# Kernel optimization log

Hardware: AMD Instinct MI355X
Metric: run time of the kernel (lower is better)

## Reference

```python
import jax, jax.numpy as jnp
import numpy as np

EMBED_DIM = 256
NUM_EMBEDDINGS = 1024
COMMITMENT_COST = 0.25


def setup_inputs() -> dict:
    key = jax.random.key(0)
    k1, k2 = jax.random.split(key)
    z_e = jax.random.normal(k1, (64, 32, 32, EMBED_DIM), dtype=jnp.float32)
    # variance_scaling(fan_in, uniform) ~ U(-sqrt(3/fan_in), sqrt(3/fan_in))
    lim = float(np.sqrt(3.0 / EMBED_DIM))
    codebook = jax.random.uniform(k2, (NUM_EMBEDDINGS, EMBED_DIM), dtype=jnp.float32,
                                  minval=-lim, maxval=lim)
    return {"z_e": z_e, "codebook": codebook}


def reference(z_e, codebook):
    codebook = jnp.asarray(codebook, dtype=jnp.float32)
    z_flat = jnp.reshape(z_e, (-1, codebook.shape[1]))  # [N, D]
    # ||z||^2 - 2 z.c + ||c||^2 -> [N, K]
    distances = (jnp.sum(z_flat ** 2, axis=1, keepdims=True)
                 - 2.0 * jnp.dot(z_flat, codebook.T)
                 + jnp.sum(codebook ** 2, axis=1))
    encoding_indices = jnp.argmin(distances, axis=1)  # [N]
    quantized = jnp.reshape(codebook[encoding_indices], z_e.shape)
    commitment_loss = COMMITMENT_COST * jnp.mean((jax.lax.stop_gradient(quantized) - z_e) ** 2)
    embedding_loss = jnp.mean((quantized - jax.lax.stop_gradient(z_e)) ** 2)
    quantized = z_e + jax.lax.stop_gradient(quantized - z_e)  # straight-through
    return (quantized, commitment_loss, embedding_loss, encoding_indices)
```

## Files before the change

### kernel.cpp

```cpp
#include <hip/hip_runtime.h>

#define NROWS  65536
#define DIM    256
#define KCB    1024
#define DELTA  0.012f
#define DELTA2 2.0e-4f
#define NRMAX  65536

typedef __attribute__((ext_vector_type(8))) _Float16 v8h;
typedef __attribute__((ext_vector_type(4))) float v4f;
typedef __attribute__((ext_vector_type(4))) int   v4i;

__device__ __forceinline__ unsigned short h16(float x) {
  _Float16 h = (_Float16)x;
  return __builtin_bit_cast(unsigned short, h);
}
__device__ __forceinline__ unsigned pk2h(float a, float b) {
  return (unsigned)h16(a) | ((unsigned)h16(b) << 16);
}
__device__ __forceinline__ v4i pk8h(float4 a, float4 b) {
  v4i r; r.x = (int)pk2h(a.x,a.y); r.y = (int)pk2h(a.z,a.w);
  r.z = (int)pk2h(b.x,b.y); r.w = (int)pk2h(b.z,b.w);
  return r;
}
__device__ __forceinline__ float f16f(float x) { return (float)(_Float16)x; }
__device__ __forceinline__ void gld16(const void* g, void* l) {
  __builtin_amdgcn_global_load_lds(
      (const __attribute__((address_space(1))) unsigned int*)g,
      (__attribute__((address_space(3))) unsigned int*)l, 16, 0, 0);
}

__global__ __launch_bounds__(256) void prep_kernel(const float* __restrict__ cb,
                                                   float* __restrict__ cnorm,
                                                   unsigned short* __restrict__ cbh,
                                                   unsigned short* __restrict__ cbl,
                                                   int* __restrict__ cnt,
                                                   int* __restrict__ cnt2) {
  int g = blockIdx.x * 256 + threadIdx.x;
  if (g == 0) { *cnt = 0; *cnt2 = 0; }
  int k = g >> 2, q = g & 3;
  int nt = k >> 7, c = k & 127;
  const float4* row = reinterpret_cast<const float4*>(cb + (size_t)k * DIM) + q * 16;
  size_t off = (size_t)((nt * 4 + q) * 128 + c) * 64;
  unsigned short* dh = cbh + off;
  unsigned short* dl = cbl + off;
  int xr = (c & 7) << 3;
  double s = 0.0;
#pragma unroll
  for (int i = 0; i < 8; ++i) {
    float4 a = row[2 * i], b = row[2 * i + 1];
    s += (double)a.x * a.x + (double)a.y * a.y + (double)a.z * a.z + (double)a.w * a.w;
    s += (double)b.x * b.x + (double)b.y * b.y + (double)b.z * b.z + (double)b.w * b.w;
    *(v4i*)(dh + ((i * 8) ^ xr)) = pk8h(a, b);
    float4 ar, br;
    ar.x = a.x - f16f(a.x); ar.y = a.y - f16f(a.y);
    ar.z = a.z - f16f(a.z); ar.w = a.w - f16f(a.w);
    br.x = b.x - f16f(b.x); br.y = b.y - f16f(b.y);
    br.z = b.z - f16f(b.z); br.w = b.w - f16f(b.w);
    *(v4i*)(dl + ((i * 8) ^ xr)) = pk8h(ar, br);
  }
  s += __shfl_xor(s, 1);
  s += __shfl_xor(s, 2);
  if (q == 0) cnorm[k] = (float)s;
}

__global__ __launch_bounds__(256, 2) void vq_mfma(
    const float* __restrict__ z, const unsigned short* __restrict__ cbh,
    const float* __restrict__ cnw, int* __restrict__ idx_arr,
    int* __restrict__ list, int* __restrict__ cnt) {
  __shared__ __align__(16) short S[32768];

  const int t = threadIdx.x;
  const int l = t & 63;
  const int w = t >> 6;
  const int l15 = l & 15, lhi = l >> 4;
  const int wm = w * 32;
  const int r0 = blockIdx.x * 128;

#pragma unroll
  for (int p = 0; p < 16; ++p) {
    int u = t + p * 256;
    int row = u >> 5, k8 = u & 31;
    const float4* s = (const float4*)(z + (size_t)(r0 + row) * DIM + k8 * 8);
    float4 a = s[0], b = s[1];
    *(v4i*)(S + row * 256 + ((k8 * 8) ^ ((row & 7) << 3))) = pk8h(a, b);
  }
  __syncthreads();

  v8h A[2][8];
#pragma unroll
  for (int mf = 0; mf < 2; ++mf) {
    int arow = wm + mf * 16 + l15;
    int base = arow * 256, xr = (arow & 7) << 3;
#pragma unroll
    for (int ks8 = 0; ks8 < 8; ++ks8)
      A[mf][ks8] = *(const v8h*)(S + base + ((ks8 * 32 + lhi * 8) ^ xr));
  }
  __syncthreads();

  auto stageC = [&](int p) {
    const char* gb = (const char*)cbh + (size_t)p * 32768 + w * 8192 + l * 16;
    char* lb = (char*)(S + (p & 1) * 16384) + w * 8192;
#pragma unroll
    for (int j = 0; j < 8; ++j) gld16(gb + j * 1024, lb + j * 1024);
  };

  int bcode[8], boff[8], bxr[8];
#pragma unroll
  for (int nf = 0; nf < 8; ++nf) {
    bcode[nf] = nf * 16 + l15;
    boff[nf] = bcode[nf] * 64;
    bxr[nf] = (bcode[nf] & 7) << 3;
  }

  float m1[8], m2[8]; int i1[8];
#pragma unroll
  for (int sl = 0; sl < 8; ++sl) { m1[sl] = 3.0e38f; m2[sl] = 3.0e38f; i1[sl] = 0; }

  stageC(0);
  __syncthreads();

  for (int nt = 0; nt < 8; ++nt) {
    float cnv[8];
#pragma unroll
    for (int nf = 0; nf < 8; ++nf) cnv[nf] = cnw[nt * 128 + bcode[nf]];

    v4f acc[2][8];
#pragma unroll
    for (int mf = 0; mf < 2; ++mf)
#pragma unroll
      for (int nf = 0; nf < 8; ++nf) acc[mf][nf] = (v4f){0.f, 0.f, 0.f, 0.f};

    for (int kh = 0; kh < 2; ++kh) {
      int p = nt * 2 + kh;
      if (p < 15) stageC(p + 1);
      const short* cur = S + (p & 1) * 16384;
#pragma unroll
      for (int ks = 0; ks < 4; ++ks) {
        int sub = (ks >> 1) * 8192;
        int ko = (ks & 1) * 32 + lhi * 8;
        v8h b[8];
#pragma unroll
        for (int nf = 0; nf < 8; ++nf)
          b[nf] = *(const v8h*)(cur + sub + boff[nf] + (ko ^ bxr[nf]));
#pragma unroll
        for (int mf = 0; mf < 2; ++mf)
#pragma unroll
          for (int nf = 0; nf < 8; ++nf)
            acc[mf][nf] = __builtin_amdgcn_mfma_f32_16x16x32_f16(A[mf][kh * 4 + ks], b[nf], acc[mf][nf], 0, 0, 0);
      }
      __syncthreads();
    }

#pragma unroll
    for (int mf = 0; mf < 2; ++mf)
#pragma unroll
      for (int nf = 0; nf < 8; ++nf) {
        int code = nt * 128 + bcode[nf];
#pragma unroll
        for (int r = 0; r < 4; ++r) {
          float s = fmaf(-2.f, acc[mf][nf][r], cnv[nf]);
          int sl = mf * 4 + r;
          m2[sl] = fminf(m2[sl], fmaxf(m1[sl], s));
          bool lt = s < m1[sl];
          i1[sl] = lt ? code : i1[sl];
          m1[sl] = lt ? s : m1[sl];
        }
      }
  }

#pragma unroll
  for (int off = 1; off < 16; off <<= 1) {
#pragma unroll
    for (int sl = 0; sl < 8; ++sl) {
      float o1 = __shfl_xor(m1[sl], off);
      int   oi = __shfl_xor(i1[sl], off);
      float o2 = __shfl_xor(m2[sl], off);
      bool bb = (o1 < m1[sl]) || (o1 == m1[sl] && oi < i1[sl]);
      float hi = fmaxf(m1[sl], o1);
      m2[sl] = fminf(hi, fminf(m2[sl], o2));
      m1[sl] = bb ? o1 : m1[sl];
      i1[sl] = bb ? oi : i1[sl];
    }
  }

  if (l15 == 0) {
#pragma unroll
    for (int sl = 0; sl < 8; ++sl) {
      int row = wm + (sl >> 2) * 16 + lhi * 4 + (sl & 3);
      idx_arr[r0 + row] = i1[sl];
      if (m2[sl] - m1[sl] < DELTA) {
        int p = atomicAdd(cnt, 1);
        list[p] = r0 + row;
      }
    }
  }
}

__global__ __launch_bounds__(256, 1) void vq_refine(
    const float* __restrict__ z,
    const unsigned short* __restrict__ cbh, const unsigned short* __restrict__ cbl,
    const float* __restrict__ cnw, const int* __restrict__ list,
    const int* __restrict__ cnt,
    float* __restrict__ pm1, float* __restrict__ pm2, int* __restrict__ pi1) {
  __shared__ __align__(16) short Ch[2][8192];
  __shared__ __align__(16) short Cl[2][8192];
  __shared__ int rows_s[64];

  const int t = threadIdx.x;
  const int l = t & 63, w = t >> 6;
  const int l15 = l & 15, lhi = l >> 4;
  const int n = *cnt;
  const int ngroups = (n + 63) >> 6;
  const int cq = blockIdx.x & 3;

  auto stage2 = [&](int g, int buf) {
    size_t go = (size_t)g * 16384 + w * 4096 + l * 16;
    char* lh = (char*)Ch[buf] + w * 4096;
    char* ll = (char*)Cl[buf] + w * 4096;
#pragma unroll
    for (int j = 0; j < 4; ++j) gld16((const char*)cbh + go + j * 1024, lh + j * 1024);
#pragma unroll
    for (int j = 0; j < 4; ++j) gld16((const char*)cbl + go + j * 1024, ll + j * 1024);
  };

  const int bxr = (l15 & 7) << 3;

  for (int grp = blockIdx.x >> 2; grp < ngroups; grp += (gridDim.x >> 2)) {
    int base = grp * 64;
    __syncthreads();
    if (t < 64) rows_s[t] = list[min(base + t, n - 1)];
    __syncthreads();
    int rowg = rows_s[w * 16 + l15];

    v8h Ah[8], Al[8];
#pragma unroll
    for (int ks8 = 0; ks8 < 8; ++ks8) {
      const float* p = z + (size_t)rowg * 256 + ks8 * 32 + lhi * 8;
      float4 a = *(const float4*)p, b = *(const float4*)(p + 4);
      v8h hv, lv;
      hv[0] = (_Float16)a.x; lv[0] = (_Float16)(a.x - (float)hv[0]);
      hv[1] = (_Float16)a.y; lv[1] = (_Float16)(a.y - (float)hv[1]);
      hv[2] = (_Float16)a.z; lv[2] = (_Float16)(a.z - (float)hv[2]);
      hv[3] = (_Float16)a.w; lv[3] = (_Float16)(a.w - (float)hv[3]);
      hv[4] = (_Float16)b.x; lv[4] = (_Float16)(b.x - (float)hv[4]);
      hv[5] = (_Float16)b.y; lv[5] = (_Float16)(b.y - (float)hv[5]);
      hv[6] = (_Float16)b.z; lv[6] = (_Float16)(b.z - (float)hv[6]);
      hv[7] = (_Float16)b.w; lv[7] = (_Float16)(b.w - (float)hv[7]);
      Ah[ks8] = hv; Al[ks8] = lv;
    }

    stage2(cq * 8, 0);
    __syncthreads();

    float m1[4], m2[4]; int i1[4];
#pragma unroll
    for (int r = 0; r < 4; ++r) { m1[r] = 3.0e38f; m2[r] = 3.0e38f; i1[r] = 0; }

#pragma unroll
    for (int tnt = 0; tnt < 2; ++tnt) {
      int nt = cq * 2 + tnt;
      float cnv[8];
#pragma unroll
      for (int nf = 0; nf < 8; ++nf) cnv[nf] = cnw[nt * 128 + nf * 16 + l15];

      v4f acc[8];
#pragma unroll
      for (int nf = 0; nf < 8; ++nf) acc[nf] = (v4f){0.f, 0.f, 0.f, 0.f};

      for (int kc = 0; kc < 4; ++kc) {
        int ph = tnt * 4 + kc;
        int g = nt * 4 + kc;
        if (ph < 7) stage2(g + 1, (ph + 1) & 1);
        const short* ch = Ch[ph & 1];
        const short* cl = Cl[ph & 1];
#pragma unroll
        for (int ks = 0; ks < 2; ++ks) {
          int ko = (ks * 32 + lhi * 8) ^ bxr;
          v8h bh[8], bl8[8];
#pragma unroll
          for (int nf = 0; nf < 8; ++nf) {
            int bo = (nf * 16 + l15) * 64 + ko;
            bh[nf]  = *(const v8h*)(ch + bo);
            bl8[nf] = *(const v8h*)(cl + bo);
          }
          v8h ah = Ah[kc * 2 + ks], al = Al[kc * 2 + ks];
#pragma unroll
          for (int nf = 0; nf < 8; ++nf) {
            acc[nf] = __builtin_amdgcn_mfma_f32_16x16x32_f16(al, bh[nf], acc[nf], 0, 0, 0);
            acc[nf] = __builtin_amdgcn_mfma_f32_16x16x32_f16(ah, bl8[nf], acc[nf], 0, 0, 0);
            acc[nf] = __builtin_amdgcn_mfma_f32_16x16x32_f16(ah, bh[nf], acc[nf], 0, 0, 0);
          }
        }
        __syncthreads();
      }

#pragma unroll
      for (int nf = 0; nf < 8; ++nf) {
        int code = nt * 128 + nf * 16 + l15;
#pragma unroll
        for (int r = 0; r < 4; ++r) {
          float s = fmaf(-2.f, acc[nf][r], cnv[nf]);
          m2[r] = fminf(m2[r], fmaxf(m1[r], s));
          bool lt = s < m1[r];
          i1[r] = lt ? code : i1[r];
          m1[r] = lt ? s : m1[r];
        }
      }
    }

#pragma unroll
    for (int off = 1; off < 16; off <<= 1) {
#pragma unroll
      for (int r = 0; r < 4; ++r) {
        float o1 = __shfl_xor(m1[r], off);
        int   oi = __shfl_xor(i1[r], off);
        float o2 = __shfl_xor(m2[r], off);
        bool bb = (o1 < m1[r]) || (o1 == m1[r] && oi < i1[r]);
        float hi = fmaxf(m1[r], o1);
        m2[r] = fminf(hi, fminf(m2[r], o2));
        m1[r] = bb ? o1 : m1[r];
        i1[r] = bb ? oi : i1[r];
      }
    }

    if (l15 == 0) {
#pragma unroll
      for (int r = 0; r < 4; ++r) {
        int fr = w * 16 + lhi * 4 + r;
        int pos = base + fr;
        if (pos < n) {
          pm1[cq * NRMAX + pos] = m1[r];
          pm2[cq * NRMAX + pos] = m2[r];
          pi1[cq * NRMAX + pos] = i1[r];
        }
      }
    }
  }
}

__global__ __launch_bounds__(256) void vq_merge(
    const int* __restrict__ list, const int* __restrict__ cnt,
    const float* __restrict__ pm1, const float* __restrict__ pm2,
    const int* __restrict__ pi1, int* __restrict__ idx_arr,
    int* __restrict__ list2, int* __restrict__ cnt2) {
  int i = blockIdx.x * 256 + threadIdx.x;
  int n = *cnt;
  if (i >= n) return;
  float m1 = pm1[i], m2 = pm2[i];
  int   i1 = pi1[i];
#pragma unroll
  for (int cq = 1; cq < 4; ++cq) {
    float o1 = pm1[cq * NRMAX + i];
    float o2 = pm2[cq * NRMAX + i];
    int   oi = pi1[cq * NRMAX + i];
    bool bb = (o1 < m1) || (o1 == m1 && oi < i1);
    float hi = fmaxf(m1, o1);
    m2 = fminf(hi, fminf(m2, o2));
    m1 = bb ? o1 : m1;
    i1 = bb ? oi : i1;
  }
  int row = list[i];
  idx_arr[row] = i1;
  if (m2 - m1 < DELTA2) {
    int p = atomicAdd(cnt2, 1);
    list2[p] = row;
  }
}

__global__ __launch_bounds__(256) void vq_rescue(
    const float* __restrict__ z, const float* __restrict__ cb,
    const float* __restrict__ cnw, const int* __restrict__ list,
    const int* __restrict__ cnt, int* __restrict__ idx_arr) {
  __shared__ float zs[256];
  __shared__ float As;
  __shared__ float wmin[4];
  __shared__ int   widx[4];

  const int t = threadIdx.x;
  const int l = t & 63, w = t >> 6;
  const int n = *cnt;

  for (int i = blockIdx.x; i < n; i += gridDim.x) {
    int row = list[i];
    __syncthreads();
    if (t < 64) ((float4*)zs)[t] = ((const float4*)(z + (size_t)row * DIM))[t];
    __syncthreads();
    if (t < 4) {
      double s = 0.0;
      const float* zz = zs + t * 64;
      for (int d = 0; d < 64; ++d) { float v = zz[d]; s += (double)v * v; }
      s += __shfl_xor(s, 1);
      s += __shfl_xor(s, 2);
      if (t == 0) As = (float)s;
    }
    __syncthreads();
    float Af = As;

    const float4* c0 = (const float4*)(cb + (size_t)(t      ) * DIM);
    const float4* c1 = (const float4*)(cb + (size_t)(t + 256) * DIM);
    const float4* c2 = (const float4*)(cb + (size_t)(t + 512) * DIM);
    const float4* c3 = (const float4*)(cb + (size_t)(t + 768) * DIM);
    float a0 = 0.f, a1 = 0.f, a2 = 0.f, a3 = 0.f;
    for (int d4 = 0; d4 < 64; ++d4) {
      float4 zq = *(const float4*)(zs + d4 * 4);
      float4 va = c0[d4], vb = c1[d4], vc = c2[d4], vd = c3[d4];
      a0 = fmaf(zq.x, va.x, a0); a0 = fmaf(zq.y, va.y, a0);
      a0 = fmaf(zq.z, va.z, a0); a0 = fmaf(zq.w, va.w, a0);
      a1 = fmaf(zq.x, vb.x, a1); a1 = fmaf(zq.y, vb.y, a1);
      a1 = fmaf(zq.z, vb.z, a1); a1 = fmaf(zq.w, vb.w, a1);
      a2 = fmaf(zq.x, vc.x, a2); a2 = fmaf(zq.y, vc.y, a2);
      a2 = fmaf(zq.z, vc.z, a2); a2 = fmaf(zq.w, vc.w, a2);
      a3 = fmaf(zq.x, vd.x, a3); a3 = fmaf(zq.y, vd.y, a3);
      a3 = fmaf(zq.z, vd.z, a3); a3 = fmaf(zq.w, vd.w, a3);
    }
    float accs[4] = {a0, a1, a2, a3};
    float mv = 3.0e38f; int mi = 0;
#pragma unroll
    for (int j = 0; j < 4; ++j) {
      int code = t + j * 256;
      float t1 = fmaf(-2.f, accs[j], Af);
      float t2 = t1 + cnw[code];
      if (t2 < mv) { mv = t2; mi = code; }
    }
#pragma unroll
    for (int off = 1; off < 64; off <<= 1) {
      float ov = __shfl_xor(mv, off);
      int   oi = __shfl_xor(mi, off);
      if (ov < mv || (ov == mv && oi < mi)) { mv = ov; mi = oi; }
    }
    if (l == 0) { wmin[w] = mv; widx[w] = mi; }
    __syncthreads();
    if (t == 0) {
      float bm = wmin[0]; int bi = widx[0];
#pragma unroll
      for (int q = 1; q < 4; ++q)
        if (wmin[q] < bm || (wmin[q] == bm && widx[q] < bi)) { bm = wmin[q]; bi = widx[q]; }
      idx_arr[row] = bi;
    }
    __syncthreads();
  }
}

__global__ __launch_bounds__(256) void vq_epilogue(
    const float* __restrict__ z, const float* __restrict__ cb,
    const int* __restrict__ idx_arr, float* __restrict__ out_q,
    float* __restrict__ out_idx, double* __restrict__ partial) {
  __shared__ int idxs[16];
  __shared__ double lw[4];
  const int t = threadIdx.x;
  const int b0 = blockIdx.x * 16;
  if (t < 16) {
    int k = idx_arr[b0 + t];
    idxs[t] = k;
    out_idx[b0 + t] = (float)k;
  }
  __syncthreads();
  const float4* zb = (const float4*)(z + (size_t)b0 * DIM);
  float4* qb = (float4*)(out_q + (size_t)b0 * DIM);
  double ls = 0.0;
#pragma unroll
  for (int p = 0; p < 4; ++p) {
    int fi = p * 256 + t;
    int ki = idxs[fi >> 6];
    float4 zv = zb[fi];
    float4 cv = ((const float4*)(cb + (size_t)ki * DIM))[fi & 63];
    float dx = cv.x - zv.x, dy = cv.y - zv.y, dz = cv.z - zv.z, dw = cv.w - zv.w;
    float4 o; o.x = zv.x + dx; o.y = zv.y + dy; o.z = zv.z + dz; o.w = zv.w + dw;
    qb[fi] = o;
    ls += (double)dx * dx + (double)dy * dy + (double)dz * dz + (double)dw * dw;
  }
#pragma unroll
  for (int off = 1; off < 64; off <<= 1) ls += __shfl_xor(ls, off);
  if ((t & 63) == 0) lw[t >> 6] = ls;
  __syncthreads();
  if (t == 0) partial[blockIdx.x] = lw[0] + lw[1] + lw[2] + lw[3];
}

__global__ __launch_bounds__(256) void finalize_kernel(const double* __restrict__ partial,
                                                       float* __restrict__ out_losses) {
  __shared__ double lw[4];
  const int t = threadIdx.x;
  double s = 0.0;
  for (int i = t; i < 4096; i += 256) s += partial[i];
#pragma unroll
  for (int off = 1; off < 64; off <<= 1) s += __shfl_xor(s, off);
  if ((t & 63) == 0) lw[t >> 6] = s;
  __syncthreads();
  if (t == 0) {
    double mse = (lw[0] + lw[1] + lw[2] + lw[3]) / ((double)NROWS * (double)DIM);
    out_losses[0] = (float)(0.25 * mse);
    out_losses[1] = (float)mse;
  }
}

extern "C" void kernel_launch(void* const* d_in, const int* in_sizes, int n_in,
                              void* d_out, int out_size, void* d_ws, size_t ws_size,
                              hipStream_t stream) {
  const float* z  = (const float*)d_in[0];
  const float* cb = (const float*)d_in[1];
  float* out = (float*)d_out;

  char* ws = (char*)d_ws;
  int*            cnt     = (int*)(ws + 0);
  int*            cnt2    = (int*)(ws + 8);
  float*          cnorm   = (float*)(ws + 4096);
  double*         partial = (double*)(ws + 8192);
  int*            idx_arr = (int*)(ws + 40960);
  int*            list    = (int*)(ws + 303104);
  int*            list2   = (int*)(ws + 565248);
  unsigned short* cbh     = (unsigned short*)(ws + 827392);
  unsigned short* cbl     = (unsigned short*)(ws + 1351680);
  float*          pm1     = (float*)(ws + 1875968);
  float*          pm2     = (float*)(ws + 2924544);
  int*            pi1     = (int*)(ws + 3973120);

  float* out_q      = out;
  float* out_losses = out + 16777216;
  float* out_idx    = out + 16777218;

  prep_kernel<<<16, 256, 0, stream>>>(cb, cnorm, cbh, cbl, cnt, cnt2);
  vq_mfma<<<NROWS / 128, 256, 0, stream>>>(z, cbh, cnorm, idx_arr, list, cnt);
  vq_refine<<<1024, 256, 0, stream>>>(z, cbh, cbl, cnorm, list, cnt, pm1, pm2, pi1);
  vq_merge<<<NRMAX / 256, 256, 0, stream>>>(list, cnt, pm1, pm2, pi1, idx_arr, list2, cnt2);
  vq_rescue<<<256, 256, 0, stream>>>(z, cb, cnorm, list2, cnt2, idx_arr);
  vq_epilogue<<<NROWS / 16, 256, 0, stream>>>(z, cb, idx_arr, out_q, out_idx, partial);
  finalize_kernel<<<1, 256, 0, stream>>>(partial, out_losses);
}
```

Before: 145.6 us.

## Triple-buffer codebook staging with finer chunks and single barrier per step

Replaces the double-buffered codebook staging (32KB chunks, two syncthreads per step) with a three-slot ring of 16KB chunks, prefetched two steps ahead. Each step is guarded by an explicit vmcnt wait plus one s_barrier. Codebook norms are preloaded into shared memory once instead of read from global memory each tile. The aim is to hide global-to-LDS latency and cut barrier stalls. In exchange it adds more LDS usage and relies on hand-written waitcnt counts matching the number of outstanding loads.

```diff
diff --git a/kernel.cpp b/kernel.cpp
--- a/kernel.cpp
+++ b/kernel.cpp
@@ -96,13 +96,20 @@
     for (int ks8 = 0; ks8 < 8; ++ks8)
       A[mf][ks8] = *(const v8h*)(S + base + ((ks8 * 32 + lhi * 8) ^ xr));
   }
+  float cn4[4];
+#pragma unroll
+  for (int j = 0; j < 4; ++j) cn4[j] = cnw[t + j * 256];
   __syncthreads();
 
-  auto stageC = [&](int p) {
-    const char* gb = (const char*)cbh + (size_t)p * 32768 + w * 8192 + l * 16;
-    char* lb = (char*)(S + (p & 1) * 16384) + w * 8192;
-#pragma unroll
-    for (int j = 0; j < 8; ++j) gld16(gb + j * 1024, lb + j * 1024);
+  float* CNS = (float*)(S + 24576);
+#pragma unroll
+  for (int j = 0; j < 4; ++j) CNS[t + j * 256] = cn4[j];
+
+  auto stageC = [&](int g) {
+    const char* gb = (const char*)cbh + (size_t)g * 16384 + w * 4096 + l * 16;
+    char* lb = (char*)S + (g % 3) * 16384 + w * 4096 + l * 16;
+#pragma unroll
+    for (int j = 0; j < 4; ++j) gld16(gb + j * 1024, lb + j * 1024);
   };
 
   int bcode[8], boff[8], bxr[8];
@@ -117,39 +124,38 @@
 #pragma unroll
   for (int sl = 0; sl < 8; ++sl) { m1[sl] = 3.0e38f; m2[sl] = 3.0e38f; i1[sl] = 0; }
 
-  stageC(0);
   __syncthreads();
+  stageC(0); stageC(1);
+
+  v4f acc[2][8];
 
   for (int nt = 0; nt < 8; ++nt) {
-    float cnv[8];
-#pragma unroll
-    for (int nf = 0; nf < 8; ++nf) cnv[nf] = cnw[nt * 128 + bcode[nf]];
-
-    v4f acc[2][8];
 #pragma unroll
     for (int mf = 0; mf < 2; ++mf)
 #pragma unroll
       for (int nf = 0; nf < 8; ++nf) acc[mf][nf] = (v4f){0.f, 0.f, 0.f, 0.f};
 
-    for (int kh = 0; kh < 2; ++kh) {
-      int p = nt * 2 + kh;
-      if (p < 15) stageC(p + 1);
-      const short* cur = S + (p & 1) * 16384;
-#pragma unroll
-      for (int ks = 0; ks < 4; ++ks) {
-        int sub = (ks >> 1) * 8192;
-        int ko = (ks & 1) * 32 + lhi * 8;
+    for (int kc = 0; kc < 4; ++kc) {
+      int g = nt * 4 + kc;
+      if (g < 31) asm volatile("s_waitcnt vmcnt(4)" ::: "memory");
+      else        asm volatile("s_waitcnt vmcnt(0)" ::: "memory");
+      __builtin_amdgcn_s_barrier();
+      __builtin_amdgcn_sched_barrier(0);
+      if (g + 2 < 32) stageC(g + 2);
+      const short* cur = S + (g % 3) * 8192;
+#pragma unroll
+      for (int ks = 0; ks < 2; ++ks) {
+        int ko = ks * 32 + lhi * 8;
         v8h b[8];
 #pragma unroll
         for (int nf = 0; nf < 8; ++nf)
-          b[nf] = *(const v8h*)(cur + sub + boff[nf] + (ko ^ bxr[nf]));
+          b[nf] = *(const v8h*)(cur + boff[nf] + (ko ^ bxr[nf]));
 #pragma unroll
         for (int mf = 0; mf < 2; ++mf)
 #pragma unroll
           for (int nf = 0; nf < 8; ++nf)
-            acc[mf][nf] = __builtin_amdgcn_mfma_f32_16x16x32_f16(A[mf][kh * 4 + ks], b[nf], acc[mf][nf], 0, 0, 0);
-      }
-      __syncthreads();
+            acc[mf][nf] = __builtin_amdgcn_mfma_f32_16x16x32_f16(A[mf][kc * 2 + ks], b[nf], acc[mf][nf], 0, 0, 0);
+      }
     }
 
 #pragma unroll
@@ -157,9 +163,10 @@
 #pragma unroll
       for (int nf = 0; nf < 8; ++nf) {
         int code = nt * 128 + bcode[nf];
+        float cn = CNS[nt * 128 + bcode[nf]];
 #pragma unroll
         for (int r = 0; r < 4; ++r) {
-          float s = fmaf(-2.f, acc[mf][nf][r], cnv[nf]);
+          float s = fmaf(-2.f, acc[mf][nf][r], cn);
           int sl = mf * 4 + r;
           m2[sl] = fminf(m2[sl], fmaxf(m1[sl], s));
           bool lt = s < m1[sl];
```

Result: no change. 146.1 us (+0.3%).
